# Optimization experiments

Hardware: AMD Instinct MI355X
Metric: run time of the kernel (lower is better)

## Reference

```python
import jax, jax.numpy as jnp
import numpy as np


def _square_distance(src, dst):
    # src: [B,N,C], dst: [B,M,C] -> [B,N,M] squared euclidean distances
    # ||s-d||^2 = -2 s.d + ||s||^2 + ||d||^2
    d = -2.0 * jnp.einsum('bnc,bmc->bnm', src, dst)
    d = d + jnp.sum(src * src, axis=-1)[:, :, None]
    d = d + jnp.sum(dst * dst, axis=-1)[:, None, :]
    return d


def setup_inputs() -> dict:
    key = jax.random.key(0)
    k1, k2 = jax.random.split(key)
    B, N, M, C = 8, 4096, 4096, 3
    f = jax.random.normal(k1, (B, N, C), dtype=jnp.float32)
    f_ = jax.random.normal(k2, (B, M, C), dtype=jnp.float32)
    return {"f": f, "f_": f_}


def reference(f, f_):
    dis = _square_distance(f, f_)          # [B,N,M]
    f2f_ = jnp.min(dis, axis=2)            # [B,N] nearest in f_ for each f point
    f_2f = jnp.min(dis, axis=1)            # [B,M] nearest in f for each f_ point
    d = jnp.mean(f2f_, axis=1) + jnp.mean(f_2f, axis=1)  # [B]
    return jnp.mean(d)
```

## Files before the change

### kernel.cpp

```cpp
#include <hip/hip_runtime.h>


typedef __attribute__((ext_vector_type(8))) short bf16x8;
typedef __attribute__((ext_vector_type(4))) float f32x4;

constexpr int B = 8;
constexpr int N = 4096;
constexpr int M = 4096;

constexpr int ROWS_PER_BLOCK = 128;
constexpr int COL_CHUNK = 2048;
constexpr int SEG = 512;
constexpr int SEGS = COL_CHUNK / SEG;
constexpr int CTILES = SEG / 16;

static __device__ __forceinline__ unsigned short f2bf(float v) {
    unsigned u = __float_as_uint(v);
    return (unsigned short)((u + 0x7FFFu + ((u >> 16) & 1u)) >> 16);
}
static __device__ __forceinline__ float bf2f(unsigned short b) {
    return __uint_as_float(((unsigned)b) << 16);
}
static __device__ __forceinline__ void split3(float v, unsigned short& a,
                                              unsigned short& b, unsigned short& c) {
    a = f2bf(v); float r = v - bf2f(a);
    b = f2bf(r); r -= bf2f(b);
    c = f2bf(r);
}

__global__ __launch_bounds__(256, 2) void chamfer_mfma_kernel(
    const float* __restrict__ f,
    const float* __restrict__ f_,
    unsigned int* __restrict__ minA,
    unsigned int* __restrict__ minB)
{
    __shared__ unsigned short Bv[SEG][32];
    __shared__ unsigned int cmin[COL_CHUNK];

    const int tid  = threadIdx.x;
    const int lane = tid & 63;
    const int w    = tid >> 6;
    const int r    = lane & 15;
    const int kg   = lane >> 4;

    const int b  = blockIdx.y;
    const int rc = blockIdx.x >> 1;
    const int cc = blockIdx.x & 1;

    for (int i = tid; i < COL_CHUNK; i += 256) cmin[i] = 0xFFFFFFFFu;

    const int rowbase = rc * ROWS_PER_BLOCK + w * 32;
    bf16x8 a0, a1;
    #pragma unroll
    for (int rt = 0; rt < 2; ++rt) {
        const float* qp = f + ((size_t)b * N + rowbase + rt * 16 + r) * 3;
        const float x = qp[0], y = qp[1], z = qp[2];
        unsigned short px0,px1,px2, py0,py1,py2, pz0,pz1,pz2, n0,n1,n2;
        split3(-2.f * x, px0, px1, px2);
        split3(-2.f * y, py0, py1, py2);
        split3(-2.f * z, pz0, pz1, pz2);
        split3(x*x + y*y + z*z, n0, n1, n2);
        const short ONE = 0x3F80;
        bf16x8 a;
        if (kg == 0)
            a = (bf16x8){(short)px0,(short)px0,(short)px1,(short)px1,(short)px0,(short)px2,(short)py0,(short)py0};
        else if (kg == 1)
            a = (bf16x8){(short)py1,(short)py1,(short)py0,(short)py2,(short)pz0,(short)pz0,(short)pz1,(short)pz1};
        else if (kg == 2)
            a = (bf16x8){(short)pz0,(short)pz2,(short)n0,(short)n1,(short)n2,ONE,ONE,ONE};
        else
            a = (bf16x8){0,0,0,0,0,0,0,0};
        if (rt == 0) a0 = a; else a1 = a;
    }

    float rm0[4], rm1[4];
    #pragma unroll
    for (int j = 0; j < 4; ++j) { rm0[j] = 3.402823466e+38f; rm1[j] = 3.402823466e+38f; }

    const float* tbase = f_ + ((size_t)b * M + (size_t)cc * COL_CHUNK) * 3;
    const bf16x8* bunits = reinterpret_cast<const bf16x8*>(&Bv[0][0]);
    const f32x4 zero = {0.f, 0.f, 0.f, 0.f};

    for (int s = 0; s < SEGS; ++s) {
        __syncthreads();
        #pragma unroll
        for (int h = 0; h < 2; ++h) {
            const int t = h * 256 + tid;
            const float* tp = tbase + (size_t)(s * SEG + t) * 3;
            const float x = tp[0], y = tp[1], z = tp[2];
            unsigned short x0,x1,x2, y0,y1,y2, z0,z1,z2, m0,m1,m2;
            split3(x, x0, x1, x2);
            split3(y, y0, y1, y2);
            split3(z, z0, z1, z2);
            split3(x*x + y*y + z*z, m0, m1, m2);
            const short ONE = 0x3F80;
            bf16x8* dst = reinterpret_cast<bf16x8*>(&Bv[t][0]);
            dst[0] = (bf16x8){(short)x0,(short)x1,(short)x0,(short)x1,(short)x2,(short)x0,(short)y0,(short)y1};
            dst[1] = (bf16x8){(short)y0,(short)y1,(short)y2,(short)y0,(short)z0,(short)z1,(short)z0,(short)z1};
            dst[2] = (bf16x8){(short)z2,(short)z0,ONE,ONE,ONE,(short)m0,(short)m1,(short)m2};
            dst[3] = (bf16x8){0,0,0,0,0,0,0,0};
        }
        __syncthreads();

        bf16x8 bb = bunits[r * 4 + kg];
        #pragma unroll 4
        for (int ct = 0; ct < CTILES; ++ct) {
            const int nct = (ct + 1) & (CTILES - 1);
            bf16x8 nb = bunits[r * 4 + kg + nct * 64];
            f32x4 c0 = __builtin_amdgcn_mfma_f32_16x16x32_bf16(a0, bb, zero, 0, 0, 0);
            f32x4 c1 = __builtin_amdgcn_mfma_f32_16x16x32_bf16(a1, bb, zero, 0, 0, 0);
            #pragma unroll
            for (int j = 0; j < 4; ++j) {
                rm0[j] = fminf(rm0[j], c0[j]);
                rm1[j] = fminf(rm1[j], c1[j]);
            }
            float v = fminf(fminf(fminf(c0[0], c0[1]), fminf(c0[2], c0[3])),
                            fminf(fminf(c1[0], c1[1]), fminf(c1[2], c1[3])));
            v = fminf(v, __shfl_xor(v, 16));
            v = fminf(v, __shfl_xor(v, 32));
            if (lane < 16)
                atomicMin(&cmin[s * SEG + ct * 16 + lane], __float_as_uint(v));
            bb = nb;
        }
    }

    #pragma unroll
    for (int rt = 0; rt < 2; ++rt) {
        #pragma unroll
        for (int j = 0; j < 4; ++j) {
            float v = rt ? rm1[j] : rm0[j];
            v = fminf(v, __shfl_xor(v, 1));
            v = fminf(v, __shfl_xor(v, 2));
            v = fminf(v, __shfl_xor(v, 4));
            v = fminf(v, __shfl_xor(v, 8));
            if (r == 0) {
                const int row = rowbase + rt * 16 + kg * 4 + j;
                atomicMin(&minA[b * N + row], __float_as_uint(v));
            }
        }
    }
    __syncthreads();
    for (int i = tid; i < COL_CHUNK; i += 256)
        atomicMin(&minB[b * M + cc * COL_CHUNK + i], cmin[i]);
}

__global__ __launch_bounds__(256) void reduce_out_kernel(
    const uint4* __restrict__ mins,
    float* __restrict__ out)
{
    __shared__ float wsum[4];
    const int tid = threadIdx.x;
    const uint4 v = mins[blockIdx.x * 256 + tid];
    float s = (__uint_as_float(v.x) + __uint_as_float(v.y))
            + (__uint_as_float(v.z) + __uint_as_float(v.w));

    #pragma unroll
    for (int off = 32; off > 0; off >>= 1) s += __shfl_down(s, off, 64);
    if ((tid & 63) == 0) wsum[tid >> 6] = s;
    __syncthreads();
    if (tid == 0) {
        const float r = (wsum[0] + wsum[1]) + (wsum[2] + wsum[3]);
        atomicAdd(out, r * (1.0f / 32768.0f));
    }
}

extern "C" void kernel_launch(void* const* d_in, const int* in_sizes, int n_in,
                              void* d_out, int out_size, void* d_ws, size_t ws_size,
                              hipStream_t stream) {
    (void)in_sizes; (void)n_in; (void)out_size; (void)ws_size;
    const float* f  = (const float*)d_in[0];
    const float* f_ = (const float*)d_in[1];
    float* out = (float*)d_out;

    unsigned int* minA = (unsigned int*)d_ws;
    unsigned int* minB = minA + (size_t)B * N;

    dim3 grid(64, 8);
    chamfer_mfma_kernel<<<grid, 256, 0, stream>>>(f, f_, minA, minB);

    reduce_out_kernel<<<64, 256, 0, stream>>>((const uint4*)minA, out);
}
```

Before: 87.22 us.

## Compute each chamfer direction separately instead of fused column-min atomics

Replaces the single pass that tracked both row minima and column minima (through per-tile shuffles and LDS atomicMin) with two independent directional passes selected by blockIdx.z. Each block now covers all M targets for its 128 query rows and only keeps register row minima. The LDS tile is rearranged into a fragment-contiguous layout so each lane reads consecutive entries. This doubles the MFMA work but removes the shuffle, LDS-atomic and global-atomic overhead from the inner loop. The grid keeps the same block count (32x8x2).

```diff
diff --git a/kernel.cpp b/kernel.cpp
--- a/kernel.cpp
+++ b/kernel.cpp
@@ -9,10 +9,9 @@
 constexpr int M = 4096;
 
 constexpr int ROWS_PER_BLOCK = 128;
-constexpr int COL_CHUNK = 2048;
-constexpr int SEG = 512;
-constexpr int SEGS = COL_CHUNK / SEG;
-constexpr int CTILES = SEG / 16;
+constexpr int SEG = 1024;
+constexpr int SEGS = M / SEG;
+constexpr int TILES = SEG / 16;
 
 static __device__ __forceinline__ unsigned short f2bf(float v) {
     unsigned u = __float_as_uint(v);
@@ -28,14 +27,13 @@
     c = f2bf(r);
 }
 
-__global__ __launch_bounds__(256, 2) void chamfer_mfma_kernel(
+__global__ __launch_bounds__(256, 2) void chamfer_dir_mfma(
     const float* __restrict__ f,
     const float* __restrict__ f_,
     unsigned int* __restrict__ minA,
     unsigned int* __restrict__ minB)
 {
-    __shared__ unsigned short Bv[SEG][32];
-    __shared__ unsigned int cmin[COL_CHUNK];
+    __shared__ bf16x8 Bt[TILES * 64];
 
     const int tid  = threadIdx.x;
     const int lane = tid & 63;
@@ -43,17 +41,19 @@
     const int r    = lane & 15;
     const int kg   = lane >> 4;
 
-    const int b  = blockIdx.y;
-    const int rc = blockIdx.x >> 1;
-    const int cc = blockIdx.x & 1;
+    const int dir = blockIdx.z;
+    const int b   = blockIdx.y;
+    const int rc  = blockIdx.x;
 
-    for (int i = tid; i < COL_CHUNK; i += 256) cmin[i] = 0xFFFFFFFFu;
+    const float* qsrc = dir ? f_ : f;
+    const float* tsrc = dir ? f  : f_;
+    unsigned int* omin = dir ? minB : minA;
 
     const int rowbase = rc * ROWS_PER_BLOCK + w * 32;
-    bf16x8 a0, a1;
+    bf16x8 afrag[2];
     #pragma unroll
     for (int rt = 0; rt < 2; ++rt) {
-        const float* qp = f + ((size_t)b * N + rowbase + rt * 16 + r) * 3;
+        const float* qp = qsrc + ((size_t)b * N + rowbase + rt * 16 + r) * 3;
         const float x = qp[0], y = qp[1], z = qp[2];
         unsigned short px0,px1,px2, py0,py1,py2, pz0,pz1,pz2, n0,n1,n2;
         split3(-2.f * x, px0, px1, px2);
@@ -70,23 +70,22 @@
             a = (bf16x8){(short)pz0,(short)pz2,(short)n0,(short)n1,(short)n2,ONE,ONE,ONE};
         else
             a = (bf16x8){0,0,0,0,0,0,0,0};
-        if (rt == 0) a0 = a; else a1 = a;
+        afrag[rt] = a;
     }
 
-    float rm0[4], rm1[4];
+    float rm[2][4];
     #pragma unroll
-    for (int j = 0; j < 4; ++j) { rm0[j] = 3.402823466e+38f; rm1[j] = 3.402823466e+38f; }
+    for (int j = 0; j < 4; ++j) { rm[0][j] = 3.402823466e+38f; rm[1][j] = 3.402823466e+38f; }
 
-    const float* tbase = f_ + ((size_t)b * M + (size_t)cc * COL_CHUNK) * 3;
-    const bf16x8* bunits = reinterpret_cast<const bf16x8*>(&Bv[0][0]);
+    const float* tb = tsrc + (size_t)b * M * 3;
     const f32x4 zero = {0.f, 0.f, 0.f, 0.f};
 
     for (int s = 0; s < SEGS; ++s) {
         __syncthreads();
         #pragma unroll
-        for (int h = 0; h < 2; ++h) {
-            const int t = h * 256 + tid;
-            const float* tp = tbase + (size_t)(s * SEG + t) * 3;
+        for (int i = 0; i < 4; ++i) {
+            const int t = i * 256 + tid;
+            const float* tp = tb + (size_t)(s * SEG + t) * 3;
             const float x = tp[0], y = tp[1], z = tp[2];
             unsigned short x0,x1,x2, y0,y1,y2, z0,z1,z2, m0,m1,m2;
             split3(x, x0, x1, x2);
@@ -94,32 +93,26 @@
             split3(z, z0, z1, z2);
             split3(x*x + y*y + z*z, m0, m1, m2);
             const short ONE = 0x3F80;
-            bf16x8* dst = reinterpret_cast<bf16x8*>(&Bv[t][0]);
-            dst[0] = (bf16x8){(short)x0,(short)x1,(short)x0,(short)x1,(short)x2,(short)x0,(short)y0,(short)y1};
-            dst[1] = (bf16x8){(short)y0,(short)y1,(short)y2,(short)y0,(short)z0,(short)z1,(short)z0,(short)z1};
-            dst[2] = (bf16x8){(short)z2,(short)z0,ONE,ONE,ONE,(short)m0,(short)m1,(short)m2};
-            dst[3] = (bf16x8){0,0,0,0,0,0,0,0};
+            const int tile = t >> 4, rr = t & 15;
+            bf16x8* base = &Bt[tile * 64 + rr];
+            base[ 0] = (bf16x8){(short)x0,(short)x1,(short)x0,(short)x1,(short)x2,(short)x0,(short)y0,(short)y1};
+            base[16] = (bf16x8){(short)y0,(short)y1,(short)y2,(short)y0,(short)z0,(short)z1,(short)z0,(short)z1};
+            base[32] = (bf16x8){(short)z2,(short)z0,ONE,ONE,ONE,(short)m0,(short)m1,(short)m2};
+            base[48] = (bf16x8){0,0,0,0,0,0,0,0};
         }
         __syncthreads();
 
-        bf16x8 bb = bunits[r * 4 + kg];
+        bf16x8 bb = Bt[lane];
         #pragma unroll 4
-        for (int ct = 0; ct < CTILES; ++ct) {
-            const int nct = (ct + 1) & (CTILES - 1);
-            bf16x8 nb = bunits[r * 4 + kg + nct * 64];
-            f32x4 c0 = __builtin_amdgcn_mfma_f32_16x16x32_bf16(a0, bb, zero, 0, 0, 0);
-            f32x4 c1 = __builtin_amdgcn_mfma_f32_16x16x32_bf16(a1, bb, zero, 0, 0, 0);
+        for (int ct = 0; ct < TILES; ++ct) {
+            bf16x8 nb = Bt[((ct + 1) & (TILES - 1)) * 64 + lane];
+            f32x4 c0 = __builtin_amdgcn_mfma_f32_16x16x32_bf16(afrag[0], bb, zero, 0, 0, 0);
+            f32x4 c1 = __builtin_amdgcn_mfma_f32_16x16x32_bf16(afrag[1], bb, zero, 0, 0, 0);
             #pragma unroll
             for (int j = 0; j < 4; ++j) {
-                rm0[j] = fminf(rm0[j], c0[j]);
-                rm1[j] = fminf(rm1[j], c1[j]);
+                rm[0][j] = fminf(rm[0][j], c0[j]);
+                rm[1][j] = fminf(rm[1][j], c1[j]);
             }
-            float v = fminf(fminf(fminf(c0[0], c0[1]), fminf(c0[2], c0[3])),
-                            fminf(fminf(c1[0], c1[1]), fminf(c1[2], c1[3])));
-            v = fminf(v, __shfl_xor(v, 16));
-            v = fminf(v, __shfl_xor(v, 32));
-            if (lane < 16)
-                atomicMin(&cmin[s * SEG + ct * 16 + lane], __float_as_uint(v));
             bb = nb;
         }
     }
@@ -128,20 +121,17 @@
     for (int rt = 0; rt < 2; ++rt) {
         #pragma unroll
         for (int j = 0; j < 4; ++j) {
-            float v = rt ? rm1[j] : rm0[j];
+            float v = rm[rt][j];
             v = fminf(v, __shfl_xor(v, 1));
             v = fminf(v, __shfl_xor(v, 2));
             v = fminf(v, __shfl_xor(v, 4));
             v = fminf(v, __shfl_xor(v, 8));
             if (r == 0) {
                 const int row = rowbase + rt * 16 + kg * 4 + j;
-                atomicMin(&minA[b * N + row], __float_as_uint(v));
+                atomicMin(&omin[b * N + row], __float_as_uint(v));
             }
         }
     }
-    __syncthreads();
-    for (int i = tid; i < COL_CHUNK; i += 256)
-        atomicMin(&minB[b * M + cc * COL_CHUNK + i], cmin[i]);
 }
 
 __global__ __launch_bounds__(256) void reduce_out_kernel(
@@ -175,8 +165,8 @@
     unsigned int* minA = (unsigned int*)d_ws;
     unsigned int* minB = minA + (size_t)B * N;
 
-    dim3 grid(64, 8);
-    chamfer_mfma_kernel<<<grid, 256, 0, stream>>>(f, f_, minA, minB);
+    dim3 grid(N / ROWS_PER_BLOCK, B, 2);
+    chamfer_dir_mfma<<<grid, 256, 0, stream>>>(f, f_, minA, minB);
 
     reduce_out_kernel<<<64, 256, 0, stream>>>((const uint4*)minA, out);
 }
```

Result: faster. 74.36 us (-14.7%).
